# Kernel optimization log

Measured on AMD Instinct MI355X. Metric: run time of the kernel, lower is better.

The kernel has to match this reference:

```python
import jax, jax.numpy as jnp
import numpy as np

B, S, H, D = 1, 4096, 16, 128
CAUSAL = True

def setup_inputs() -> dict:
    key = jax.random.key(0)
    kq, kk, kv = jax.random.split(key, 3)
    query = jax.random.normal(kq, (B, S, H, D), dtype=jnp.float32)
    k = jax.random.normal(kk, (B, S, H, D), dtype=jnp.float32)
    v = jax.random.normal(kv, (B, S, H, D), dtype=jnp.float32)
    return {"query": query, "key": k, "value": v}

def _attention(q, k, v):
    # q,k,v: [B, S, H, D] (flash-attn layout). Ulysses all2all + ring attention
    # compose to exact global attention; single-device reference is plain SDPA.
    scale = 1.0 / jnp.sqrt(jnp.asarray(q.shape[-1], q.dtype))
    scores = jnp.einsum("bshd,bthd->bhst", q, k) * scale  # [B,H,S,S]
    if CAUSAL:
        s = q.shape[1]
        mask = jnp.tril(jnp.ones((s, s), dtype=bool))
        scores = jnp.where(mask, scores, jnp.finfo(scores.dtype).min)
    probs = jax.nn.softmax(scores, axis=-1)
    return jnp.einsum("bhst,bthd->bshd", probs, v)

def reference(query, key, value):
    return _attention(query, key, value)
```

## Files before the change

kernel.cpp:

```cpp
#include <hip/hip_runtime.h>
#include <hip/hip_bf16.h>

typedef __bf16 bf16x8 __attribute__((ext_vector_type(8)));
typedef __bf16 bf16x4 __attribute__((ext_vector_type(4)));
typedef float  f32x4  __attribute__((ext_vector_type(4)));

#define SEQ   4096
#define NH    16
#define HD    128
#define KVB   32
#define NT32  128
#define STR   (NH * HD)
#define TE    4096
#define WSK   ((size_t)NH * NT32 * TE)
#define MASKV -3.0e38f

__device__ __forceinline__ bf16x8 cvt_bf16x8(f32x4 a, f32x4 b, float s) {
    bf16x8 v;
    v[0] = (__bf16)(a[0]*s); v[1] = (__bf16)(a[1]*s);
    v[2] = (__bf16)(a[2]*s); v[3] = (__bf16)(a[3]*s);
    v[4] = (__bf16)(b[0]*s); v[5] = (__bf16)(b[1]*s);
    v[6] = (__bf16)(b[2]*s); v[7] = (__bf16)(b[3]*s);
    return v;
}

__global__ __launch_bounds__(256) void prep_kernel(
    const float* __restrict__ K, const float* __restrict__ V, __bf16* __restrict__ ws)
{
    const int tid = threadIdx.x;
    const int bid = blockIdx.x;
    const int h   = bid >> 7;
    const int t   = bid & 127;

    __bf16* kimg = ws + (size_t)(h*NT32 + t) * TE;
    __bf16* vimg = ws + WSK + (size_t)(h*NT32 + t) * TE;

    const int row = tid >> 3;
    #pragma unroll
    for (int u = 0; u < 2; ++u) {
        const int ch = (tid & 7)*2 + u;
        const float* src = K + (size_t)(t*KVB + row)*STR + h*HD + ch*8;
        f32x4 a = *(const f32x4*)src;
        f32x4 b = *(const f32x4*)(src + 4);
        const int e = (row*HD + ch*8) ^ ((row & 7) << 3);
        *(bf16x8*)&kimg[e] = cvt_bf16x8(a, b, 1.0f);
    }

    const int d4 = (tid & 31) * 4;
    const int pl = (tid >> 5) & 3;
    const int ih = tid >> 7;
    f32x4 va[4];
    #pragma unroll
    for (int r = 0; r < 4; ++r) {
        const int kr = t*KVB + 16*ih + 4*pl + r;
        va[r] = *(const f32x4*)(V + (size_t)kr*STR + h*HD + d4);
    }
    #pragma unroll
    for (int i4 = 0; i4 < 4; ++i4) {
        const int d = d4 + i4;
        bf16x4 w;
        w[0] = (__bf16)va[0][i4]; w[1] = (__bf16)va[1][i4];
        w[2] = (__bf16)va[2][i4]; w[3] = (__bf16)va[3][i4];
        const int e = d*KVB + 8*(pl ^ ((d >> 1) & 3)) + 4*ih;
        *(bf16x4*)&vimg[e] = w;
    }
}

__global__ __launch_bounds__(512) void fattn7_kernel(
    const float* __restrict__ Q, const __bf16* __restrict__ ws, float* __restrict__ O)
{
    __shared__ __align__(16) char ldsraw[66048];

    const int tid  = threadIdx.x;
    const int lane = tid & 63;
    const int wv   = tid >> 6;
    const int grp  = wv >> 2;
    const int wg   = wv & 3;
    const int c    = lane & 15;
    const int g    = lane >> 4;

    const int bid = blockIdx.x;
    const int h   = bid & 15;
    const int j   = bid >> 4;

    const __bf16* kws = ws;
    const __bf16* vws = ws + WSK;
    float* ml = (float*)(ldsraw + 65536);

    #define ISSUE(TT, BUF)  do {                                                       \
        const size_t tb_ = (size_t)(h*NT32 + (TT)) * TE;                               \
        _Pragma("unroll")                                                              \
        for (int ci = 0; ci < 4; ++ci) {                                               \
            const int fb = (4*wg + ci) * 1024;                                         \
            const __bf16* src = (fb < 8192) ? (kws + tb_ + (fb >> 1) + lane*8)         \
                                            : (vws + tb_ + ((fb - 8192) >> 1) + lane*8); \
            __builtin_amdgcn_global_load_lds(                                          \
                (const __attribute__((address_space(1))) void*)src,                    \
                (__attribute__((address_space(3))) void*)(ldsraw + grp*32768 + (BUF)*16384 + fb), \
                16, 0, 0);                                                             \
        }                                                                              \
    } while (0)

    const float scale = 0.08838834764831845f * 1.4426950408889634f;

    for (int ph = 0; ph < 2; ++ph) {
        const int qb   = ph ? j : (31 - j);
        const int q0   = qb * 128;
        const int qlo0 = q0 + 32*wg;
        const int nst  = 2*qb + 2;
        const int tb0  = grp * nst;

        bf16x8 qf[2][4];
        #pragma unroll
        for (int sub = 0; sub < 2; ++sub) {
            const float* qrow = Q + (size_t)(qlo0 + 16*sub + c) * STR + h*HD;
            #pragma unroll
            for (int ks = 0; ks < 4; ++ks) {
                const int d0 = 32*ks + 8*g;
                qf[sub][ks] = cvt_bf16x8(*(const f32x4*)(qrow + d0), *(const f32x4*)(qrow + d0 + 4), scale);
            }
        }

        f32x4 oacc[2][8];
        #pragma unroll
        for (int s2 = 0; s2 < 2; ++s2)
            #pragma unroll
            for (int i = 0; i < 8; ++i) { oacc[s2][i][0]=0.f; oacc[s2][i][1]=0.f; oacc[s2][i][2]=0.f; oacc[s2][i][3]=0.f; }
        float lrow[2] = {0.f, 0.f};

        int buf = 0;
        ISSUE(tb0, 0);

        for (int t = 0; t < nst; ++t) {
            __syncthreads();
            if (t + 1 < nst) ISSUE(tb0 + t + 1, buf ^ 1);

            const int k0 = (tb0 + t) * KVB;
            if (k0 <= qlo0 + 47) {
                const __bf16* bK = (const __bf16*)(ldsraw + grp*32768 + buf*16384);
                const __bf16* bV = bK + 4096;

                f32x4 s[2][2];
                #pragma unroll
                for (int a = 0; a < 2; ++a)
                    #pragma unroll
                    for (int b = 0; b < 2; ++b) { s[a][b][0]=0.f; s[a][b][1]=0.f; s[a][b][2]=0.f; s[a][b][3]=0.f; }
                __builtin_amdgcn_s_setprio(1);
                #pragma unroll
                for (int ks = 0; ks < 4; ++ks) {
                    const int e0 = (c*HD + 32*ks + 8*g) ^ ((c & 7) << 3);
                    bf16x8 ak0 = *(const bf16x8*)&bK[e0];
                    bf16x8 ak1 = *(const bf16x8*)&bK[e0 + 16*HD];
                    s[0][0] = __builtin_amdgcn_mfma_f32_16x16x32_bf16(ak0, qf[0][ks], s[0][0], 0, 0, 0);
                    s[0][1] = __builtin_amdgcn_mfma_f32_16x16x32_bf16(ak1, qf[0][ks], s[0][1], 0, 0, 0);
                    s[1][0] = __builtin_amdgcn_mfma_f32_16x16x32_bf16(ak0, qf[1][ks], s[1][0], 0, 0, 0);
                    s[1][1] = __builtin_amdgcn_mfma_f32_16x16x32_bf16(ak1, qf[1][ks], s[1][1], 0, 0, 0);
                }
                __builtin_amdgcn_s_setprio(0);

                if (k0 + 31 > qlo0) {
                    #pragma unroll
                    for (int sub = 0; sub < 2; ++sub) {
                        const int qg = qlo0 + 16*sub + c;
                        #pragma unroll
                        for (int r = 0; r < 4; ++r) {
                            if (k0 + 4*g + r > qg)      s[sub][0][r] = MASKV;
                            if (k0 + 16 + 4*g + r > qg) s[sub][1][r] = MASKV;
                        }
                    }
                }

                bf16x8 pa[2];
                #pragma unroll
                for (int sub = 0; sub < 2; ++sub) {
                    float rs = 0.f;
                    #pragma unroll
                    for (int r = 0; r < 4; ++r) {
                        s[sub][0][r] = exp2f(s[sub][0][r]); rs += s[sub][0][r];
                        s[sub][1][r] = exp2f(s[sub][1][r]); rs += s[sub][1][r];
                    }
                    lrow[sub] += rs;
                    pa[sub][0]=(__bf16)s[sub][0][0]; pa[sub][1]=(__bf16)s[sub][0][1];
                    pa[sub][2]=(__bf16)s[sub][0][2]; pa[sub][3]=(__bf16)s[sub][0][3];
                    pa[sub][4]=(__bf16)s[sub][1][0]; pa[sub][5]=(__bf16)s[sub][1][1];
                    pa[sub][6]=(__bf16)s[sub][1][2]; pa[sub][7]=(__bf16)s[sub][1][3];
                }

                __builtin_amdgcn_s_setprio(1);
                #pragma unroll
                for (int dt = 0; dt < 8; ++dt) {
                    const int d = 16*dt + c;
                    const int e = d*KVB + ((8*g) ^ (((d >> 1) & 3) << 3));
                    bf16x8 bv = *(const bf16x8*)&bV[e];
                    oacc[0][dt] = __builtin_amdgcn_mfma_f32_16x16x32_bf16(pa[0], bv, oacc[0][dt], 0, 0, 0);
                    oacc[1][dt] = __builtin_amdgcn_mfma_f32_16x16x32_bf16(pa[1], bv, oacc[1][dt], 0, 0, 0);
                }
                __builtin_amdgcn_s_setprio(0);
            }
            buf ^= 1;
        }

        #pragma unroll
        for (int sub = 0; sub < 2; ++sub) {
            lrow[sub] += __shfl_xor(lrow[sub], 16, 64);
            lrow[sub] += __shfl_xor(lrow[sub], 32, 64);
        }

        __syncthreads();
        float* dump = (float*)ldsraw;
        if (grp == 1) {
            #pragma unroll
            for (int sub = 0; sub < 2; ++sub) {
                if (lane < 16) ml[32*wg + 16*sub + c] = lrow[sub];
                #pragma unroll
                for (int dt = 0; dt < 8; ++dt)
                    #pragma unroll
                    for (int r = 0; r < 4; ++r)
                        dump[(32*wg + 16*sub + 4*g + r)*128 + 16*dt + c] = oacc[sub][dt][r];
            }
        }
        __syncthreads();
        if (grp == 0) {
            #pragma unroll
            for (int sub = 0; sub < 2; ++sub) {
                const int ql = 32*wg + 16*sub;
                const float inv = 1.0f / (lrow[sub] + ml[ql + c]);
                #pragma unroll
                for (int r = 0; r < 4; ++r) {
                    const float cv = __shfl(inv, 20*g + r, 64);
                    float* orow = O + (size_t)(q0 + ql + 4*g + r)*STR + h*HD;
                    #pragma unroll
                    for (int dt = 0; dt < 8; ++dt)
                        orow[16*dt + c] = (oacc[sub][dt][r] + dump[(ql + 4*g + r)*128 + 16*dt + c]) * cv;
                }
            }
        }
        __syncthreads();
    }
    #undef ISSUE
}

extern "C" void kernel_launch(void* const* d_in, const int* in_sizes, int n_in,
                              void* d_out, int out_size, void* d_ws, size_t ws_size,
                              hipStream_t stream) {
    const float* Q = (const float*)d_in[0];
    const float* K = (const float*)d_in[1];
    const float* V = (const float*)d_in[2];
    float* O = (float*)d_out;

    prep_kernel<<<dim3(NH * NT32), dim3(256), 0, stream>>>(K, V, (__bf16*)d_ws);
    fattn7_kernel<<<dim3(16 * NH), dim3(512), 0, stream>>>(Q, (const __bf16*)d_ws, O);
}
```

Measured before the change: 126.6 us.

## Quad-buffer KV tiles in LDS and process two tiles per barrier

```diff
diff --git a/kernel.cpp b/kernel.cpp
--- a/kernel.cpp
+++ b/kernel.cpp
@@ -66,10 +66,10 @@
     }
 }
 
-__global__ __launch_bounds__(512) void fattn7_kernel(
+__global__ __launch_bounds__(512) void fattn9_kernel(
     const float* __restrict__ Q, const __bf16* __restrict__ ws, float* __restrict__ O)
 {
-    __shared__ __align__(16) char ldsraw[66048];
+    __shared__ __align__(16) char ldsraw[131584];
 
     const int tid  = threadIdx.x;
     const int lane = tid & 63;
@@ -85,7 +85,7 @@
 
     const __bf16* kws = ws;
     const __bf16* vws = ws + WSK;
-    float* ml = (float*)(ldsraw + 65536);
+    float* ml = (float*)(ldsraw + 131072);
 
     #define ISSUE(TT, BUF)  do {                                                       \
         const size_t tb_ = (size_t)(h*NT32 + (TT)) * TE;                               \
@@ -96,8 +96,69 @@
                                             : (vws + tb_ + ((fb - 8192) >> 1) + lane*8); \
             __builtin_amdgcn_global_load_lds(                                          \
                 (const __attribute__((address_space(1))) void*)src,                    \
-                (__attribute__((address_space(3))) void*)(ldsraw + grp*32768 + (BUF)*16384 + fb), \
+                (__attribute__((address_space(3))) void*)(ldsraw + grp*65536 + (BUF)*16384 + fb), \
                 16, 0, 0);                                                             \
+        }                                                                              \
+    } while (0)
+
+    #define STEP(T)  do {                                                              \
+        const int k0 = (tb0 + (T)) * KVB;                                              \
+        if (k0 <= qlo0 + 47) {                                                         \
+            const __bf16* bK = (const __bf16*)(ldsraw + grp*65536 + ((T) & 3)*16384);  \
+            const __bf16* bV = bK + 4096;                                              \
+            f32x4 s[2][2];                                                             \
+            _Pragma("unroll")                                                          \
+            for (int a_ = 0; a_ < 2; ++a_)                                             \
+                _Pragma("unroll")                                                      \
+                for (int b_ = 0; b_ < 2; ++b_) { s[a_][b_][0]=0.f; s[a_][b_][1]=0.f; s[a_][b_][2]=0.f; s[a_][b_][3]=0.f; } \
+            __builtin_amdgcn_s_setprio(1);                                             \
+            _Pragma("unroll")                                                          \
+            for (int ks = 0; ks < 4; ++ks) {                                           \
+                const int e0 = (c*HD + 32*ks + 8*g) ^ ((c & 7) << 3);                  \
+                bf16x8 ak0 = *(const bf16x8*)&bK[e0];                                  \
+                bf16x8 ak1 = *(const bf16x8*)&bK[e0 + 16*HD];                          \
+                s[0][0] = __builtin_amdgcn_mfma_f32_16x16x32_bf16(ak0, qf[0][ks], s[0][0], 0, 0, 0); \
+                s[0][1] = __builtin_amdgcn_mfma_f32_16x16x32_bf16(ak1, qf[0][ks], s[0][1], 0, 0, 0); \
+                s[1][0] = __builtin_amdgcn_mfma_f32_16x16x32_bf16(ak0, qf[1][ks], s[1][0], 0, 0, 0); \
+                s[1][1] = __builtin_amdgcn_mfma_f32_16x16x32_bf16(ak1, qf[1][ks], s[1][1], 0, 0, 0); \
+            }                                                                          \
+            __builtin_amdgcn_s_setprio(0);                                             \
+            if (k0 + 31 > qlo0) {                                                      \
+                _Pragma("unroll")                                                      \
+                for (int sub = 0; sub < 2; ++sub) {                                    \
+                    const int qg = qlo0 + 16*sub + c;                                  \
+                    _Pragma("unroll")                                                  \
+                    for (int r = 0; r < 4; ++r) {                                      \
+                        if (k0 + 4*g + r > qg)      s[sub][0][r] = MASKV;              \
+                        if (k0 + 16 + 4*g + r > qg) s[sub][1][r] = MASKV;              \
+                    }                                                                  \
+                }                                                                      \
+            }                                                                          \
+            bf16x8 pa[2];                                                              \
+            _Pragma("unroll")                                                          \
+            for (int sub = 0; sub < 2; ++sub) {                                        \
+                float rs = 0.f;                                                        \
+                _Pragma("unroll")                                                      \
+                for (int r = 0; r < 4; ++r) {                                          \
+                    s[sub][0][r] = exp2f(s[sub][0][r]); rs += s[sub][0][r];            \
+                    s[sub][1][r] = exp2f(s[sub][1][r]); rs += s[sub][1][r];            \
+                }                                                                      \
+                lrow[sub] += rs;                                                       \
+                pa[sub][0]=(__bf16)s[sub][0][0]; pa[sub][1]=(__bf16)s[sub][0][1];      \
+                pa[sub][2]=(__bf16)s[sub][0][2]; pa[sub][3]=(__bf16)s[sub][0][3];      \
+                pa[sub][4]=(__bf16)s[sub][1][0]; pa[sub][5]=(__bf16)s[sub][1][1];      \
+                pa[sub][6]=(__bf16)s[sub][1][2]; pa[sub][7]=(__bf16)s[sub][1][3];      \
+            }                                                                          \
+            __builtin_amdgcn_s_setprio(1);                                             \
+            _Pragma("unroll")                                                          \
+            for (int dt = 0; dt < 8; ++dt) {                                           \
+                const int d = 16*dt + c;                                               \
+                const int e = d*KVB + ((8*g) ^ (((d >> 1) & 3) << 3));                 \
+                bf16x8 bv = *(const bf16x8*)&bV[e];                                    \
+                oacc[0][dt] = __builtin_amdgcn_mfma_f32_16x16x32_bf16(pa[0], bv, oacc[0][dt], 0, 0, 0); \
+                oacc[1][dt] = __builtin_amdgcn_mfma_f32_16x16x32_bf16(pa[1], bv, oacc[1][dt], 0, 0, 0); \
+            }                                                                          \
+            __builtin_amdgcn_s_setprio(0);                                             \
         }                                                                              \
     } while (0)
 
@@ -128,76 +189,14 @@
             for (int i = 0; i < 8; ++i) { oacc[s2][i][0]=0.f; oacc[s2][i][1]=0.f; oacc[s2][i][2]=0.f; oacc[s2][i][3]=0.f; }
         float lrow[2] = {0.f, 0.f};
 
-        int buf = 0;
-        ISSUE(tb0, 0);
-
-        for (int t = 0; t < nst; ++t) {
+        ISSUE(tb0 + 0, 0);
+        ISSUE(tb0 + 1, 1);
+
+        for (int w = 0; w < nst; w += 2) {
             __syncthreads();
-            if (t + 1 < nst) ISSUE(tb0 + t + 1, buf ^ 1);
-
-            const int k0 = (tb0 + t) * KVB;
-            if (k0 <= qlo0 + 47) {
-                const __bf16* bK = (const __bf16*)(ldsraw + grp*32768 + buf*16384);
-                const __bf16* bV = bK + 4096;
-
-                f32x4 s[2][2];
-                #pragma unroll
-                for (int a = 0; a < 2; ++a)
-                    #pragma unroll
-                    for (int b = 0; b < 2; ++b) { s[a][b][0]=0.f; s[a][b][1]=0.f; s[a][b][2]=0.f; s[a][b][3]=0.f; }
-                __builtin_amdgcn_s_setprio(1);
-                #pragma unroll
-                for (int ks = 0; ks < 4; ++ks) {
-                    const int e0 = (c*HD + 32*ks + 8*g) ^ ((c & 7) << 3);
-                    bf16x8 ak0 = *(const bf16x8*)&bK[e0];
-                    bf16x8 ak1 = *(const bf16x8*)&bK[e0 + 16*HD];
-                    s[0][0] = __builtin_amdgcn_mfma_f32_16x16x32_bf16(ak0, qf[0][ks], s[0][0], 0, 0, 0);
-                    s[0][1] = __builtin_amdgcn_mfma_f32_16x16x32_bf16(ak1, qf[0][ks], s[0][1], 0, 0, 0);
-                    s[1][0] = __builtin_amdgcn_mfma_f32_16x16x32_bf16(ak0, qf[1][ks], s[1][0], 0, 0, 0);
-                    s[1][1] = __builtin_amdgcn_mfma_f32_16x16x32_bf16(ak1, qf[1][ks], s[1][1], 0, 0, 0);
-                }
-                __builtin_amdgcn_s_setprio(0);
-
-                if (k0 + 31 > qlo0) {
-                    #pragma unroll
-                    for (int sub = 0; sub < 2; ++sub) {
-                        const int qg = qlo0 + 16*sub + c;
-                        #pragma unroll
-                        for (int r = 0; r < 4; ++r) {
-                            if (k0 + 4*g + r > qg)      s[sub][0][r] = MASKV;
-                            if (k0 + 16 + 4*g + r > qg) s[sub][1][r] = MASKV;
-                        }
-                    }
-                }
-
-                bf16x8 pa[2];
-                #pragma unroll
-                for (int sub = 0; sub < 2; ++sub) {
-                    float rs = 0.f;
-                    #pragma unroll
-                    for (int r = 0; r < 4; ++r) {
-                        s[sub][0][r] = exp2f(s[sub][0][r]); rs += s[sub][0][r];
-                        s[sub][1][r] = exp2f(s[sub][1][r]); rs += s[sub][1][r];
-                    }
-                    lrow[sub] += rs;
-                    pa[sub][0]=(__bf16)s[sub][0][0]; pa[sub][1]=(__bf16)s[sub][0][1];
-                    pa[sub][2]=(__bf16)s[sub][0][2]; pa[sub][3]=(__bf16)s[sub][0][3];
-                    pa[sub][4]=(__bf16)s[sub][1][0]; pa[sub][5]=(__bf16)s[sub][1][1];
-                    pa[sub][6]=(__bf16)s[sub][1][2]; pa[sub][7]=(__bf16)s[sub][1][3];
-                }
-
-                __builtin_amdgcn_s_setprio(1);
-                #pragma unroll
-                for (int dt = 0; dt < 8; ++dt) {
-                    const int d = 16*dt + c;
-                    const int e = d*KVB + ((8*g) ^ (((d >> 1) & 3) << 3));
-                    bf16x8 bv = *(const bf16x8*)&bV[e];
-                    oacc[0][dt] = __builtin_amdgcn_mfma_f32_16x16x32_bf16(pa[0], bv, oacc[0][dt], 0, 0, 0);
-                    oacc[1][dt] = __builtin_amdgcn_mfma_f32_16x16x32_bf16(pa[1], bv, oacc[1][dt], 0, 0, 0);
-                }
-                __builtin_amdgcn_s_setprio(0);
-            }
-            buf ^= 1;
+            if (w + 2 < nst) { ISSUE(tb0 + w + 2, (w + 2) & 3); ISSUE(tb0 + w + 3, (w + 3) & 3); }
+            STEP(w);
+            STEP(w + 1);
         }
 
         #pragma unroll
@@ -238,6 +237,7 @@
         __syncthreads();
     }
     #undef ISSUE
+    #undef STEP
 }
 
 extern "C" void kernel_launch(void* const* d_in, const int* in_sizes, int n_in,
@@ -249,5 +249,5 @@
     float* O = (float*)d_out;
 
     prep_kernel<<<dim3(NH * NT32), dim3(256), 0, stream>>>(K, V, (__bf16*)d_ws);
-    fattn7_kernel<<<dim3(16 * NH), dim3(512), 0, stream>>>(Q, (const __bf16*)d_ws, O);
-}
+    fattn9_kernel<<<dim3(16 * NH), dim3(512), 0, stream>>>(Q, (const __bf16*)d_ws, O);
+}
```

Result: faster. 120.1 us, median of 6 (-5.1%).
